# Kernel optimization log

Measured on AMD Instinct MI355X. Metric: run time of the kernel, lower is better.

## Reference

```python
import jax, jax.numpy as jnp
import numpy as np

B, C, H, W = 16, 256, 32, 32
AD, SC, R = 16, 32, 4


def _conv1x1(x, w, b):
    # x: [B,Cin,H,W], w: [Cout,Cin], b: [Cout]
    return jnp.einsum('oc,bchw->bohw', w, x) + b[None, :, None, None]


def setup_inputs() -> dict:
    key = jax.random.key(0)
    ks = jax.random.split(key, 12)
    p = lambda k, shape: (jax.random.normal(k, shape, dtype=jnp.float32) * 0.02)
    return {
        'x': jax.random.normal(ks[0], (B, C, H, W), dtype=jnp.float32),
        'fc1_w': p(ks[1], (C // R, C)), 'fc1_b': jnp.zeros((C // R,), jnp.float32),
        'fc2_w': p(ks[2], (C, C // R)), 'fc2_b': jnp.zeros((C,), jnp.float32),
        'qkv_w': p(ks[3], (AD * 2 + SC, SC)), 'qkv_b': jnp.zeros((AD * 2 + SC,), jnp.float32),
        'proj_w': p(ks[4], (SC, SC)), 'proj_b': jnp.zeros((SC,), jnp.float32),
        'ffn1_w': p(ks[5], (4 * C, C)), 'ffn1_b': jnp.zeros((4 * C,), jnp.float32),
        'ffn2_w': p(ks[6], (C, 4 * C)), 'ffn2_b': jnp.zeros((C,), jnp.float32),
    }


def reference(x, fc1_w, fc1_b, fc2_w, fc2_b, qkv_w, qkv_b, proj_w, proj_b,
              ffn1_w, ffn1_b, ffn2_w, ffn2_b):
    # --- DynamicChannelSelect: SE gate then channel split ---
    s = x.mean(axis=(2, 3), keepdims=True)                       # [B,C,1,1]
    s = jax.nn.relu(_conv1x1(s, fc1_w, fc1_b))
    s = jax.nn.sigmoid(_conv1x1(s, fc2_w, fc2_b))
    xg = x * s
    attn_part, non_attn_part = xg[:, :SC], xg[:, SC:]

    # --- SHSA: single-head self-attention on SC channels ---
    qkv = _conv1x1(attn_part, qkv_w, qkv_b)                      # [B,2*AD+SC,H,W]
    q = qkv[:, :AD].reshape(B, AD, H * W)
    k = qkv[:, AD:2 * AD].reshape(B, AD, H * W)
    v = qkv[:, 2 * AD:].reshape(B, SC, H * W)
    scale = AD ** -0.5
    attn = jax.nn.softmax(jnp.einsum('bcn,bcm->bnm', q, k) * scale, axis=-1)  # [B,N,N]
    out = jnp.einsum('bcm,bnm->bcn', v, attn).reshape(B, SC, H, W)
    attn_out = _conv1x1(out, proj_w, proj_b)

    # --- concat + 1x1-conv FFN ---
    y = jnp.concatenate([attn_out, non_attn_part], axis=1)       # [B,C,H,W]
    h = jax.nn.relu(_conv1x1(y, ffn1_w, ffn1_b))                 # [B,4C,H,W]
    return _conv1x1(h, ffn2_w, ffn2_b)                           # [B,C,H,W]
```

## Files before the change

kernel.cpp:

```cpp
#include <hip/hip_runtime.h>
#include <cstdint>
#include <cstddef>

#define BB 16
#define CC 256
#define NP 1024

typedef __attribute__((ext_vector_type(8))) short bf16x8;
typedef __attribute__((ext_vector_type(4))) float f32x4;
typedef unsigned short u16;

__device__ __forceinline__ u16 f2bf(float f) {
    union { float f; uint32_t u; } v; v.f = f;
    uint32_t u = v.u;
    return (u16)((u + 0x7FFFu + ((u >> 16) & 1u)) >> 16);
}

__global__ __launch_bounds__(256)
void se_mean_conv_kernel(const float* __restrict__ x, float* __restrict__ s_mean,
                         const float* __restrict__ w1, u16* __restrict__ d1,
                         const float* __restrict__ w2, u16* __restrict__ d2) {
    int blk = blockIdx.x;
    int t = threadIdx.x;
    if (blk < BB * CC) {
        const float* p = x + (size_t)blk * NP;
        float4 v = *(const float4*)(p + t * 4);
        float s = (v.x + v.y) + (v.z + v.w);
#pragma unroll
        for (int off = 32; off; off >>= 1) s += __shfl_down(s, off, 64);
        __shared__ float red[4];
        if ((t & 63) == 0) red[t >> 6] = s;
        __syncthreads();
        if (t == 0) s_mean[blk] = (red[0] + red[1] + red[2] + red[3]) * (1.0f / NP);
    } else {
        int blk2 = blk - BB * CC;
        const float* src = (blk2 < 256) ? w1 : w2;
        u16* dst = (blk2 < 256) ? d1 : d2;
        int i = ((blk2 & 255) * 256 + t) * 4;
        float4 v = *(const float4*)(src + i);
        ushort4 o;
        o.x = f2bf(v.x); o.y = f2bf(v.y); o.z = f2bf(v.z); o.w = f2bf(v.w);
        *(ushort4*)(dst + i) = o;
    }
}

__global__ __launch_bounds__(256)
void scale_transpose_qkv_kernel(const float* __restrict__ x, const float* __restrict__ s_mean,
                                const float* __restrict__ fc1_w, const float* __restrict__ fc1_b,
                                const float* __restrict__ fc2_w, const float* __restrict__ fc2_b,
                                const float* __restrict__ qW, const float* __restrict__ qB,
                                u16* __restrict__ ygt, u16* __restrict__ Qt,
                                u16* __restrict__ Kt, u16* __restrict__ Vb) {
    int nt = blockIdx.x, ct = blockIdx.y, b = blockIdx.z;
    __shared__ float tile[64][65];
    __shared__ float ws[64 * 32];
    __shared__ float bs[64];
    __shared__ float vtile[32][64];
    __shared__ float smean_s[CC];
    __shared__ float h1[64];
    __shared__ float sig_l[64];
    int t = threadIdx.x;
    const float* Xb = x + ((size_t)b * CC + ct * 64) * NP + nt * 64;
    smean_s[t] = s_mean[b * CC + t];
    if (ct == 0) {
        for (int e = t; e < 2048; e += 256) ws[e] = qW[e];
        if (t < 64) bs[t] = qB[t];
    }
#pragma unroll
    for (int p = 0; p < 4; ++p) {
        int e = t + p * 256;
        int c = e >> 4, n4 = (e & 15) * 4;
        float4 v = *(const float4*)&Xb[(size_t)c * NP + n4];
        tile[c][n4] = v.x; tile[c][n4 + 1] = v.y; tile[c][n4 + 2] = v.z; tile[c][n4 + 3] = v.w;
    }
    __syncthreads();
    if (t < 64) {
        float a = fc1_b[t];
#pragma unroll 4
        for (int c = 0; c < CC; ++c) a += fc1_w[t * CC + c] * smean_s[c];
        h1[t] = fmaxf(a, 0.f);
    }
    __syncthreads();
    if (t < 64) {
        int c = ct * 64 + t;
        float a = fc2_b[c];
#pragma unroll 8
        for (int j = 0; j < 64; ++j) a += fc2_w[c * 64 + j] * h1[j];
        sig_l[t] = 1.f / (1.f + __expf(-a));
    }
    __syncthreads();
    u16* Yb = ygt + ((size_t)b * NP + nt * 64) * CC + ct * 64;
#pragma unroll
    for (int p = 0; p < 4; ++p) {
        int e = t + p * 256;
        int n = e >> 4, c4 = (e & 15) * 4;
        if (ct * 64 + c4 >= 32) {
            ushort4 o;
            o.x = f2bf(tile[c4][n] * sig_l[c4]);
            o.y = f2bf(tile[c4 + 1][n] * sig_l[c4 + 1]);
            o.z = f2bf(tile[c4 + 2][n] * sig_l[c4 + 2]);
            o.w = f2bf(tile[c4 + 3][n] * sig_l[c4 + 3]);
            *(ushort4*)&Yb[(size_t)n * CC + c4] = o;
        }
    }
    if (ct == 0) {
        int nn = t & 63, g = t >> 6;
        int n = nt * 64 + nn;
        float xs[32];
#pragma unroll
        for (int c = 0; c < 32; ++c) xs[c] = tile[c][nn] * sig_l[c];
        float acc[16];
#pragma unroll
        for (int oc = 0; oc < 16; ++oc) {
            int o = g * 16 + oc;
            float a = bs[o];
#pragma unroll
            for (int c = 0; c < 32; ++c) a += ws[o * 32 + c] * xs[c];
            acc[oc] = a;
        }
        if (g == 0) {
            u16* qr = Qt + ((size_t)b * NP + n) * 32;
            ushort4 z4; z4.x = 0; z4.y = 0; z4.z = 0; z4.w = 0;
#pragma unroll
            for (int j = 0; j < 16; j += 4) {
                ushort4 o4;
                o4.x = f2bf(acc[j] * 0.25f);     o4.y = f2bf(acc[j + 1] * 0.25f);
                o4.z = f2bf(acc[j + 2] * 0.25f); o4.w = f2bf(acc[j + 3] * 0.25f);
                *(ushort4*)&qr[j] = o4;
            }
            *(ushort4*)&qr[16] = z4; *(ushort4*)&qr[20] = z4;
            *(ushort4*)&qr[24] = z4; *(ushort4*)&qr[28] = z4;
        } else if (g == 1) {
            u16* kr = Kt + ((size_t)b * NP + n) * 32;
            ushort4 z4; z4.x = 0; z4.y = 0; z4.z = 0; z4.w = 0;
#pragma unroll
            for (int j = 0; j < 16; j += 4) {
                ushort4 k4;
                k4.x = f2bf(acc[j]);     k4.y = f2bf(acc[j + 1]);
                k4.z = f2bf(acc[j + 2]); k4.w = f2bf(acc[j + 3]);
                *(ushort4*)&kr[j] = k4;
            }
            *(ushort4*)&kr[16] = z4; *(ushort4*)&kr[20] = z4;
            *(ushort4*)&kr[24] = z4; *(ushort4*)&kr[28] = z4;
        } else {
#pragma unroll
            for (int oc = 0; oc < 16; ++oc) vtile[(g - 2) * 16 + oc][nn] = acc[oc];
        }
        __syncthreads();
        for (int e = t; e < 2048; e += 256) {
            int c = e >> 6, nn2 = e & 63;
            Vb[(size_t)b * 32 * NP + (size_t)c * NP + nt * 64 + nn2] = f2bf(vtile[c][nn2]);
        }
    }
}

__global__ __launch_bounds__(256)
void attn_mfma_kernel(const u16* __restrict__ Qt, const u16* __restrict__ Kt,
                      const u16* __restrict__ Vb,
                      const float* __restrict__ proj_w, const float* __restrict__ proj_b,
                      u16* __restrict__ ygt) {
    int b = blockIdx.x & 15;
    int n0 = (blockIdx.x >> 4) * 16;
    __shared__ __align__(16) u16 P_lds[4][16][40];
    __shared__ float al_lds[4][16];
    __shared__ float sm_lds[4][16];
    __shared__ float sl_lds[4][16];
    __shared__ float O_lds[4][16][33];
    __shared__ float pw_s[32][32];
    __shared__ float pb_s[32];
    int t = threadIdx.x;
    int w = t >> 6, lane = t & 63;
    int q = lane >> 4, idx = lane & 15;

    for (int e = t; e < 1024; e += 256) pw_s[e >> 5][e & 31] = proj_w[e];
    if (t < 32) pb_s[t] = proj_b[t];
    __syncthreads();

    const u16* Qb = Qt + (size_t)b * NP * 32;
    const u16* Kb = Kt + (size_t)b * NP * 32;
    const u16* Vp = Vb + (size_t)b * 32 * NP;

    int nrow = n0 + idx;
    bf16x8 aq = *(const bf16x8*)&Qb[(size_t)nrow * 32 + q * 8];

    f32x4 O0 = {0.f, 0.f, 0.f, 0.f}, O1 = {0.f, 0.f, 0.f, 0.f};
    float m_run[4] = {-1e30f, -1e30f, -1e30f, -1e30f};
    float l_run[4] = {0.f, 0.f, 0.f, 0.f};

    int mbase = w * 256;
    for (int m0 = mbase; m0 < mbase + 256; m0 += 32) {
        bf16x8 bk0 = *(const bf16x8*)&Kb[(size_t)(m0 + idx) * 32 + q * 8];
        bf16x8 bk1 = *(const bf16x8*)&Kb[(size_t)(m0 + 16 + idx) * 32 + q * 8];
        bf16x8 va0 = *(const bf16x8*)&Vp[(size_t)idx * NP + m0 + q * 8];
        bf16x8 va1 = *(const bf16x8*)&Vp[(size_t)(16 + idx) * NP + m0 + q * 8];
        f32x4 z = {0.f, 0.f, 0.f, 0.f};
        f32x4 S0 = __builtin_amdgcn_mfma_f32_16x16x32_bf16(aq, bk0, z, 0, 0, 0);
        f32x4 S1 = __builtin_amdgcn_mfma_f32_16x16x32_bf16(aq, bk1, z, 0, 0, 0);
        float mx[4], p0[4], p1[4], alpha[4];
#pragma unroll
        for (int r = 0; r < 4; ++r) mx[r] = fmaxf(S0[r], S1[r]);
#pragma unroll
        for (int off = 1; off < 16; off <<= 1)
#pragma unroll
            for (int r = 0; r < 4; ++r) mx[r] = fmaxf(mx[r], __shfl_xor(mx[r], off, 64));
#pragma unroll
        for (int r = 0; r < 4; ++r) {
            float nm = fmaxf(m_run[r], mx[r]);
            alpha[r] = __expf(m_run[r] - nm);
            m_run[r] = nm;
            p0[r] = __expf(S0[r] - nm);
            p1[r] = __expf(S1[r] - nm);
        }
#pragma unroll
        for (int r = 0; r < 4; ++r) {
            float s = p0[r] + p1[r];
#pragma unroll
            for (int off = 1; off < 16; off <<= 1) s += __shfl_xor(s, off, 64);
            l_run[r] = l_run[r] * alpha[r] + s;
        }
#pragma unroll
        for (int r = 0; r < 4; ++r) {
            P_lds[w][q * 4 + r][idx]      = f2bf(p0[r]);
            P_lds[w][q * 4 + r][idx + 16] = f2bf(p1[r]);
        }
        if (idx == 0) {
#pragma unroll
            for (int r = 0; r < 4; ++r) al_lds[w][q * 4 + r] = alpha[r];
        }
        float an = al_lds[w][idx];
#pragma unroll
        for (int r = 0; r < 4; ++r) { O0[r] *= an; O1[r] *= an; }
        bf16x8 pf = *(const bf16x8*)&P_lds[w][idx][q * 8];
        O0 = __builtin_amdgcn_mfma_f32_16x16x32_bf16(va0, pf, O0, 0, 0, 0);
        O1 = __builtin_amdgcn_mfma_f32_16x16x32_bf16(va1, pf, O1, 0, 0, 0);
    }
    if (idx == 0) {
#pragma unroll
        for (int r = 0; r < 4; ++r) {
            sm_lds[w][q * 4 + r] = m_run[r];
            sl_lds[w][q * 4 + r] = l_run[r];
        }
    }
#pragma unroll
    for (int r = 0; r < 4; ++r) {
        O_lds[w][idx][q * 4 + r]      = O0[r];
        O_lds[w][idx][q * 4 + r + 16] = O1[r];
    }
    __syncthreads();
    if (w == 0) {
        float m0_ = sm_lds[0][idx], m1 = sm_lds[1][idx], m2 = sm_lds[2][idx], m3 = sm_lds[3][idx];
        float gm = fmaxf(fmaxf(m0_, m1), fmaxf(m2, m3));
        float e0 = __expf(m0_ - gm), e1 = __expf(m1 - gm);
        float e2 = __expf(m2 - gm), e3 = __expf(m3 - gm);
        float linv = 1.f / (sl_lds[0][idx] * e0 + sl_lds[1][idx] * e1 +
                            sl_lds[2][idx] * e2 + sl_lds[3][idx] * e3);
#pragma unroll
        for (int r = 0; r < 4; ++r) {
            int c0 = q * 4 + r;
            O_lds[0][idx][c0] = (O_lds[0][idx][c0] * e0 + O_lds[1][idx][c0] * e1 +
                                 O_lds[2][idx][c0] * e2 + O_lds[3][idx][c0] * e3) * linv;
            int c1 = c0 + 16;
            O_lds[0][idx][c1] = (O_lds[0][idx][c1] * e0 + O_lds[1][idx][c1] * e1 +
                                 O_lds[2][idx][c1] * e2 + O_lds[3][idx][c1] * e3) * linv;
        }
        float o0[4], o1[4];
#pragma unroll
        for (int r = 0; r < 4; ++r) { o0[r] = pb_s[q * 4 + r]; o1[r] = pb_s[q * 4 + r + 16]; }
#pragma unroll
        for (int c = 0; c < 32; ++c) {
            float xv = O_lds[0][idx][c];
#pragma unroll
            for (int r = 0; r < 4; ++r) {
                o0[r] += pw_s[q * 4 + r][c] * xv;
                o1[r] += pw_s[q * 4 + r + 16][c] * xv;
            }
        }
        u16* yrow = ygt + ((size_t)b * NP + n0 + idx) * CC;
        ushort4 w0, w1;
        w0.x = f2bf(o0[0]); w0.y = f2bf(o0[1]); w0.z = f2bf(o0[2]); w0.w = f2bf(o0[3]);
        w1.x = f2bf(o1[0]); w1.y = f2bf(o1[1]); w1.z = f2bf(o1[2]); w1.w = f2bf(o1[3]);
        *(ushort4*)&yrow[q * 4] = w0;
        *(ushort4*)&yrow[q * 4 + 16] = w1;
    }
}

template <int K>
__global__ __launch_bounds__(256)
void mfma_gemm_kernel(const u16* __restrict__ A, const u16* __restrict__ Bt,
                      const float* __restrict__ bias, u16* __restrict__ Y, int M) {
    __shared__ __align__(16) u16 As[2][128][64];
    __shared__ __align__(16) u16 Bs[2][128][64];
    constexpr int NIT = K / 64;
    int id = blockIdx.x;
    int xcd = id & 7, qq = id >> 3;
    int mt = qq >> 4;
    int nt = ((qq & 15) << 3) | xcd;
    const u16* Ab = A + (size_t)mt * 128 * K;
    const u16* Bb = Bt + (size_t)nt * 128 * K;
    int t = threadIdx.x;
    int w = t >> 6, lane = t & 63;
    int q = lane >> 4, idx = lane & 15;
    int wr = (w >> 1) * 64, wc = (w & 1) * 64;
    int srow = lane >> 3;
    int gch = (lane & 7) ^ srow;

    f32x4 acc[4][4];
#pragma unroll
    for (int i = 0; i < 4; ++i)
#pragma unroll
        for (int j = 0; j < 4; ++j) { f32x4 z = {0.f, 0.f, 0.f, 0.f}; acc[i][j] = z; }

#define ISSUE_LOADS(buf, k0)                                                              \
    {                                                                                     \
        _Pragma("unroll")                                                                 \
        for (int p = 0; p < 4; ++p) {                                                     \
            int r = w * 32 + p * 8 + srow;                                                \
            __builtin_amdgcn_global_load_lds(                                             \
                (const __attribute__((address_space(1))) void*)(Ab + (size_t)r * K + (k0) + gch * 8), \
                (__attribute__((address_space(3))) void*)(&As[buf][w * 32 + p * 8][0]),   \
                16, 0, 0);                                                                \
        }                                                                                 \
        _Pragma("unroll")                                                                 \
        for (int p = 0; p < 4; ++p) {                                                     \
            int r = w * 32 + p * 8 + srow;                                                \
            __builtin_amdgcn_global_load_lds(                                             \
                (const __attribute__((address_space(1))) void*)(Bb + (size_t)r * K + (k0) + gch * 8), \
                (__attribute__((address_space(3))) void*)(&Bs[buf][w * 32 + p * 8][0]),   \
                16, 0, 0);                                                                \
        }                                                                                 \
    }

    ISSUE_LOADS(0, 0)
    for (int ki = 0; ki < NIT; ++ki) {
        int cur = ki & 1;
        __syncthreads();
        if (ki + 1 < NIT) ISSUE_LOADS(cur ^ 1, (ki + 1) * 64)
#pragma unroll
        for (int h = 0; h < 2; ++h) {
            bf16x8 af[4], bfr[4];
#pragma unroll
            for (int i = 0; i < 4; ++i)
                af[i] = *(const bf16x8*)&As[cur][wr + i * 16 + idx][(((q + 4 * h) ^ (idx & 7)) * 8)];
#pragma unroll
            for (int j = 0; j < 4; ++j)
                bfr[j] = *(const bf16x8*)&Bs[cur][wc + j * 16 + idx][(((q + 4 * h) ^ (idx & 7)) * 8)];
#pragma unroll
            for (int i = 0; i < 4; ++i)
#pragma unroll
                for (int j = 0; j < 4; ++j)
                    acc[i][j] = __builtin_amdgcn_mfma_f32_16x16x32_bf16(af[i], bfr[j], acc[i][j], 0, 0, 0);
        }
    }
#undef ISSUE_LOADS

    __syncthreads();
    u16* tile = &As[0][0][0];
#pragma unroll
    for (int i = 0; i < 4; ++i) {
        int m0 = wr + i * 16 + q * 4;
        int gm = mt * 128 + m0;
        float b0 = bias[gm], b1 = bias[gm + 1], b2 = bias[gm + 2], b3 = bias[gm + 3];
        int c16 = m0 >> 3;
        int off = (q & 1) * 4;
#pragma unroll
        for (int j = 0; j < 4; ++j) {
            int nl = wc + j * 16 + idx;
            f32x4 v = acc[i][j];
            ushort4 o;
            o.x = f2bf(fmaxf(v.x + b0, 0.f)); o.y = f2bf(fmaxf(v.y + b1, 0.f));
            o.z = f2bf(fmaxf(v.z + b2, 0.f)); o.w = f2bf(fmaxf(v.w + b3, 0.f));
            int cs = c16 ^ (nl & 7);
            *(ushort4*)&tile[nl * 128 + cs * 8 + off] = o;
        }
    }
    __syncthreads();
#pragma unroll
    for (int p = 0; p < 8; ++p) {
        int flat = p * 256 + t;
        int n = flat >> 4, c = flat & 15;
        int cs = c ^ (n & 7);
        bf16x8 v = *(const bf16x8*)&tile[n * 128 + cs * 8];
        *(bf16x8*)&Y[((size_t)(nt * 128 + n)) * (size_t)M + mt * 128 + c * 8] = v;
    }
}

template <int K>
__global__ __launch_bounds__(256)
void mfma_gemm_64_kernel(const u16* __restrict__ A, const u16* __restrict__ Bt,
                         const float* __restrict__ bias, float* __restrict__ Y, int M) {
    __shared__ __align__(16) u16 As[2][64][64];
    __shared__ __align__(16) u16 Bs[2][64][64];
    constexpr int NIT = K / 64;
    int id = blockIdx.x;
    int xcd = id & 7, u = id >> 3;
    int mt = u >> 5;
    int j  = (u >> 1) & 15;
    int p_ = u & 1;
    int nt = (((j << 3) | xcd) << 1) | p_;
    const u16* Ab = A + (size_t)mt * 64 * K;
    const u16* Bb = Bt + (size_t)nt * 64 * K;
    int t = threadIdx.x;
    int w = t >> 6, lane = t & 63;
    int q = lane >> 4, idx = lane & 15;
    int wr = (w >> 1) * 32, wc = (w & 1) * 32;
    int srow = lane >> 3;
    int gch = (lane & 7) ^ srow;

    f32x4 acc[2][2];
#pragma unroll
    for (int i = 0; i < 2; ++i)
#pragma unroll
        for (int jj = 0; jj < 2; ++jj) { f32x4 z = {0.f, 0.f, 0.f, 0.f}; acc[i][jj] = z; }

#define ISSUE_LOADS64(buf, k0)                                                            \
    {                                                                                     \
        _Pragma("unroll")                                                                 \
        for (int p = 0; p < 2; ++p) {                                                     \
            int r = w * 16 + p * 8 + srow;                                                \
            __builtin_amdgcn_global_load_lds(                                             \
                (const __attribute__((address_space(1))) void*)(Ab + (size_t)r * K + (k0) + gch * 8), \
                (__attribute__((address_space(3))) void*)(&As[buf][w * 16 + p * 8][0]),   \
                16, 0, 0);                                                                \
        }                                                                                 \
        _Pragma("unroll")                                                                 \
        for (int p = 0; p < 2; ++p) {                                                     \
            int r = w * 16 + p * 8 + srow;                                                \
            __builtin_amdgcn_global_load_lds(                                             \
                (const __attribute__((address_space(1))) void*)(Bb + (size_t)r * K + (k0) + gch * 8), \
                (__attribute__((address_space(3))) void*)(&Bs[buf][w * 16 + p * 8][0]),   \
                16, 0, 0);                                                                \
        }                                                                                 \
    }

    ISSUE_LOADS64(0, 0)
    for (int ki = 0; ki < NIT; ++ki) {
        int cur = ki & 1;
        __syncthreads();
        if (ki + 1 < NIT) ISSUE_LOADS64(cur ^ 1, (ki + 1) * 64)
#pragma unroll
        for (int h = 0; h < 2; ++h) {
            bf16x8 af[2], bfr[2];
#pragma unroll
            for (int i = 0; i < 2; ++i)
                af[i] = *(const bf16x8*)&As[cur][wr + i * 16 + idx][(((q + 4 * h) ^ (idx & 7)) * 8)];
#pragma unroll
            for (int jj = 0; jj < 2; ++jj)
                bfr[jj] = *(const bf16x8*)&Bs[cur][wc + jj * 16 + idx][(((q + 4 * h) ^ (idx & 7)) * 8)];
#pragma unroll
            for (int i = 0; i < 2; ++i)
#pragma unroll
                for (int jj = 0; jj < 2; ++jj)
                    acc[i][jj] = __builtin_amdgcn_mfma_f32_16x16x32_bf16(af[i], bfr[jj], acc[i][jj], 0, 0, 0);
        }
    }
#undef ISSUE_LOADS64

#pragma unroll
    for (int i = 0; i < 2; ++i) {
        int m0 = mt * 64 + wr + i * 16 + q * 4;
        float b0 = bias[m0], b1 = bias[m0 + 1], b2 = bias[m0 + 2], b3 = bias[m0 + 3];
#pragma unroll
        for (int jj = 0; jj < 2; ++jj) {
            int ng = nt * 64 + wc + jj * 16 + idx;
            int bb = ng >> 10, nn = ng & 1023;
            f32x4 v = acc[i][jj];
            float* p = Y + ((size_t)bb * M + m0) * NP + nn;
            p[0]      = v.x + b0;
            p[NP]     = v.y + b1;
            p[2 * NP] = v.z + b2;
            p[3 * NP] = v.w + b3;
        }
    }
}

extern "C" void kernel_launch(void* const* d_in, const int* in_sizes, int n_in,
                              void* d_out, int out_size, void* d_ws, size_t ws_size,
                              hipStream_t stream) {
    const float* x      = (const float*)d_in[0];
    const float* fc1_w  = (const float*)d_in[1];
    const float* fc1_b  = (const float*)d_in[2];
    const float* fc2_w  = (const float*)d_in[3];
    const float* fc2_b  = (const float*)d_in[4];
    const float* qkv_w  = (const float*)d_in[5];
    const float* qkv_b  = (const float*)d_in[6];
    const float* proj_w = (const float*)d_in[7];
    const float* proj_b = (const float*)d_in[8];
    const float* ffn1_w = (const float*)d_in[9];
    const float* ffn1_b = (const float*)d_in[10];
    const float* ffn2_w = (const float*)d_in[11];
    const float* ffn2_b = (const float*)d_in[12];
    float* out = (float*)d_out;

    u16* w1b = (u16*)d_ws;
    u16* w2b = w1b + 262144;
    u16* ygt = w2b + 262144;
    u16* ht  = ygt + (size_t)BB * NP * CC;
    float* s_mean = (float*)ht;
    u16* Qt = (u16*)(s_mean + BB * CC);
    u16* Kt = Qt + (size_t)BB * NP * 32;
    u16* Vb = Kt + (size_t)BB * NP * 32;

    se_mean_conv_kernel<<<BB * CC + 512, 256, 0, stream>>>(x, s_mean, ffn1_w, w1b, ffn2_w, w2b);
    scale_transpose_qkv_kernel<<<dim3(16, 4, BB), 256, 0, stream>>>(
        x, s_mean, fc1_w, fc1_b, fc2_w, fc2_b, qkv_w, qkv_b, ygt, Qt, Kt, Vb);
    attn_mfma_kernel<<<BB * 64, 256, 0, stream>>>(Qt, Kt, Vb, proj_w, proj_b, ygt);

    mfma_gemm_kernel<256><<<1024, 256, 0, stream>>>(w1b, ygt, ffn1_b, ht, 1024);
    mfma_gemm_64_kernel<1024><<<1024, 256, 0, stream>>>(w2b, ht, ffn2_b, out, 256);
}
```

Baseline: 170.8 us.

## Fuse the two FFN GEMMs into one kernel keeping hidden activations in LDS

The separate FFN1 and FFN2 GEMM kernels are replaced by one fused kernel. Each block owns 64 pixels, computes the 1024-wide hidden layer in 64-channel chunks into double-buffered LDS, and accumulates the FFN2 output in registers. This removes the global write and re-read of the 32 MB bf16 hidden tensor and one launch. In exchange only 256 blocks run, weights are read straight from global/L2 into registers with no LDS staging, and each chunk needs a block barrier, so occupancy and latency hiding may suffer.

```diff
diff --git a/kernel.cpp b/kernel.cpp
--- a/kernel.cpp
+++ b/kernel.cpp
@@ -284,191 +284,112 @@
     }
 }
 
-template <int K>
 __global__ __launch_bounds__(256)
-void mfma_gemm_kernel(const u16* __restrict__ A, const u16* __restrict__ Bt,
-                      const float* __restrict__ bias, u16* __restrict__ Y, int M) {
-    __shared__ __align__(16) u16 As[2][128][64];
-    __shared__ __align__(16) u16 Bs[2][128][64];
-    constexpr int NIT = K / 64;
-    int id = blockIdx.x;
-    int xcd = id & 7, qq = id >> 3;
-    int mt = qq >> 4;
-    int nt = ((qq & 15) << 3) | xcd;
-    const u16* Ab = A + (size_t)mt * 128 * K;
-    const u16* Bb = Bt + (size_t)nt * 128 * K;
+void ffn_fused_kernel(const u16* __restrict__ w1b, const u16* __restrict__ w2b,
+                      const u16* __restrict__ ygt,
+                      const float* __restrict__ bias1, const float* __restrict__ bias2,
+                      float* __restrict__ out) {
+    __shared__ __align__(16) u16 Ys[4][64][64];
+    __shared__ __align__(16) u16 Hs[2][64][64];
+    __shared__ float Bs1[1024];
     int t = threadIdx.x;
     int w = t >> 6, lane = t & 63;
     int q = lane >> 4, idx = lane & 15;
-    int wr = (w >> 1) * 64, wc = (w & 1) * 64;
     int srow = lane >> 3;
     int gch = (lane & 7) ^ srow;
-
-    f32x4 acc[4][4];
-#pragma unroll
-    for (int i = 0; i < 4; ++i)
-#pragma unroll
-        for (int j = 0; j < 4; ++j) { f32x4 z = {0.f, 0.f, 0.f, 0.f}; acc[i][j] = z; }
-
-#define ISSUE_LOADS(buf, k0)                                                              \
-    {                                                                                     \
-        _Pragma("unroll")                                                                 \
-        for (int p = 0; p < 4; ++p) {                                                     \
-            int r = w * 32 + p * 8 + srow;                                                \
-            __builtin_amdgcn_global_load_lds(                                             \
-                (const __attribute__((address_space(1))) void*)(Ab + (size_t)r * K + (k0) + gch * 8), \
-                (__attribute__((address_space(3))) void*)(&As[buf][w * 32 + p * 8][0]),   \
-                16, 0, 0);                                                                \
-        }                                                                                 \
-        _Pragma("unroll")                                                                 \
-        for (int p = 0; p < 4; ++p) {                                                     \
-            int r = w * 32 + p * 8 + srow;                                                \
-            __builtin_amdgcn_global_load_lds(                                             \
-                (const __attribute__((address_space(1))) void*)(Bb + (size_t)r * K + (k0) + gch * 8), \
-                (__attribute__((address_space(3))) void*)(&Bs[buf][w * 32 + p * 8][0]),   \
-                16, 0, 0);                                                                \
-        }                                                                                 \
-    }
-
-    ISSUE_LOADS(0, 0)
-    for (int ki = 0; ki < NIT; ++ki) {
-        int cur = ki & 1;
+    int n0 = blockIdx.x * 64;
+
+#pragma unroll
+    for (int p = 0; p < 8; ++p) {
+        int kb = p >> 1;
+        int nb = (p & 1) * 32 + w * 8;
+        __builtin_amdgcn_global_load_lds(
+            (const __attribute__((address_space(1))) void*)(ygt + (size_t)(n0 + nb + srow) * CC + kb * 64 + gch * 8),
+            (__attribute__((address_space(3))) void*)(&Ys[kb][nb][0]),
+            16, 0, 0);
+    }
+    for (int e = t; e < 1024; e += 256) Bs1[e] = bias1[e];
+
+    f32x4 oacc[4][4];
+#pragma unroll
+    for (int f = 0; f < 4; ++f)
+#pragma unroll
+        for (int j = 0; j < 4; ++j) { f32x4 z = {0.f, 0.f, 0.f, 0.f}; oacc[f][j] = z; }
+
+    __syncthreads();
+
+    bf16x8 af[8];
+    {
+        const u16* a1 = w1b + ((size_t)(w * 16 + idx)) * CC;
+#pragma unroll
+        for (int s = 0; s < 8; ++s) af[s] = *(const bf16x8*)(a1 + s * 32 + q * 8);
+    }
+
+    for (int ch = 0; ch < 16; ++ch) {
+        bf16x8 af2[4][2];
+        const u16* a2 = w2b + ((size_t)(w * 64 + idx)) * 1024 + ch * 64;
+#pragma unroll
+        for (int f = 0; f < 4; ++f)
+#pragma unroll
+            for (int s2 = 0; s2 < 2; ++s2)
+                af2[f][s2] = *(const bf16x8*)(a2 + (size_t)f * 16 * 1024 + s2 * 32 + q * 8);
+
+        f32x4 hacc[4];
+#pragma unroll
+        for (int j = 0; j < 4; ++j) { f32x4 z = {0.f, 0.f, 0.f, 0.f}; hacc[j] = z; }
+#pragma unroll
+        for (int s = 0; s < 8; ++s) {
+            int kb = s >> 1, hh = s & 1;
+#pragma unroll
+            for (int j = 0; j < 4; ++j) {
+                bf16x8 yb = *(const bf16x8*)&Ys[kb][j * 16 + idx][(((q + 4 * hh) ^ (idx & 7)) * 8)];
+                hacc[j] = __builtin_amdgcn_mfma_f32_16x16x32_bf16(af[s], yb, hacc[j], 0, 0, 0);
+            }
+        }
+        int mbase = ch * 64 + w * 16 + q * 4;
+        float b0 = Bs1[mbase], b1v = Bs1[mbase + 1], b2v = Bs1[mbase + 2], b3v = Bs1[mbase + 3];
+        int chk_hi = w * 2 + (q >> 1);
+#pragma unroll
+        for (int j = 0; j < 4; ++j) {
+            int n = j * 16 + idx;
+            int chk = chk_hi ^ (n & 7);
+            uint32_t lo = (uint32_t)f2bf(fmaxf(hacc[j][0] + b0, 0.f)) |
+                          ((uint32_t)f2bf(fmaxf(hacc[j][1] + b1v, 0.f)) << 16);
+            uint32_t hi = (uint32_t)f2bf(fmaxf(hacc[j][2] + b2v, 0.f)) |
+                          ((uint32_t)f2bf(fmaxf(hacc[j][3] + b3v, 0.f)) << 16);
+            uint32_t* hp = (uint32_t*)&Hs[ch & 1][n][chk * 8 + (q & 1) * 4];
+            hp[0] = lo; hp[1] = hi;
+        }
         __syncthreads();
-        if (ki + 1 < NIT) ISSUE_LOADS(cur ^ 1, (ki + 1) * 64)
-#pragma unroll
-        for (int h = 0; h < 2; ++h) {
-            bf16x8 af[4], bfr[4];
-#pragma unroll
-            for (int i = 0; i < 4; ++i)
-                af[i] = *(const bf16x8*)&As[cur][wr + i * 16 + idx][(((q + 4 * h) ^ (idx & 7)) * 8)];
-#pragma unroll
-            for (int j = 0; j < 4; ++j)
-                bfr[j] = *(const bf16x8*)&Bs[cur][wc + j * 16 + idx][(((q + 4 * h) ^ (idx & 7)) * 8)];
-#pragma unroll
-            for (int i = 0; i < 4; ++i)
-#pragma unroll
-                for (int j = 0; j < 4; ++j)
-                    acc[i][j] = __builtin_amdgcn_mfma_f32_16x16x32_bf16(af[i], bfr[j], acc[i][j], 0, 0, 0);
-        }
-    }
-#undef ISSUE_LOADS
-
-    __syncthreads();
-    u16* tile = &As[0][0][0];
-#pragma unroll
-    for (int i = 0; i < 4; ++i) {
-        int m0 = wr + i * 16 + q * 4;
-        int gm = mt * 128 + m0;
-        float b0 = bias[gm], b1 = bias[gm + 1], b2 = bias[gm + 2], b3 = bias[gm + 3];
-        int c16 = m0 >> 3;
-        int off = (q & 1) * 4;
+        if (ch + 1 < 16) {
+            const u16* a1 = w1b + ((size_t)((ch + 1) * 64 + w * 16 + idx)) * CC;
+#pragma unroll
+            for (int s = 0; s < 8; ++s) af[s] = *(const bf16x8*)(a1 + s * 32 + q * 8);
+        }
+#pragma unroll
+        for (int s2 = 0; s2 < 2; ++s2)
+#pragma unroll
+            for (int j = 0; j < 4; ++j) {
+                bf16x8 hb = *(const bf16x8*)&Hs[ch & 1][j * 16 + idx][(((q + 4 * s2) ^ (idx & 7)) * 8)];
+#pragma unroll
+                for (int f = 0; f < 4; ++f)
+                    oacc[f][j] = __builtin_amdgcn_mfma_f32_16x16x32_bf16(af2[f][s2], hb, oacc[f][j], 0, 0, 0);
+            }
+    }
+
+    int b = n0 >> 10, nnb = n0 & 1023;
+#pragma unroll
+    for (int f = 0; f < 4; ++f) {
+        int m2 = w * 64 + f * 16 + q * 4;
+        float c0 = bias2[m2], c1 = bias2[m2 + 1], c2 = bias2[m2 + 2], c3 = bias2[m2 + 3];
 #pragma unroll
         for (int j = 0; j < 4; ++j) {
-            int nl = wc + j * 16 + idx;
-            f32x4 v = acc[i][j];
-            ushort4 o;
-            o.x = f2bf(fmaxf(v.x + b0, 0.f)); o.y = f2bf(fmaxf(v.y + b1, 0.f));
-            o.z = f2bf(fmaxf(v.z + b2, 0.f)); o.w = f2bf(fmaxf(v.w + b3, 0.f));
-            int cs = c16 ^ (nl & 7);
-            *(ushort4*)&tile[nl * 128 + cs * 8 + off] = o;
-        }
-    }
-    __syncthreads();
-#pragma unroll
-    for (int p = 0; p < 8; ++p) {
-        int flat = p * 256 + t;
-        int n = flat >> 4, c = flat & 15;
-        int cs = c ^ (n & 7);
-        bf16x8 v = *(const bf16x8*)&tile[n * 128 + cs * 8];
-        *(bf16x8*)&Y[((size_t)(nt * 128 + n)) * (size_t)M + mt * 128 + c * 8] = v;
-    }
-}
-
-template <int K>
-__global__ __launch_bounds__(256)
-void mfma_gemm_64_kernel(const u16* __restrict__ A, const u16* __restrict__ Bt,
-                         const float* __restrict__ bias, float* __restrict__ Y, int M) {
-    __shared__ __align__(16) u16 As[2][64][64];
-    __shared__ __align__(16) u16 Bs[2][64][64];
-    constexpr int NIT = K / 64;
-    int id = blockIdx.x;
-    int xcd = id & 7, u = id >> 3;
-    int mt = u >> 5;
-    int j  = (u >> 1) & 15;
-    int p_ = u & 1;
-    int nt = (((j << 3) | xcd) << 1) | p_;
-    const u16* Ab = A + (size_t)mt * 64 * K;
-    const u16* Bb = Bt + (size_t)nt * 64 * K;
-    int t = threadIdx.x;
-    int w = t >> 6, lane = t & 63;
-    int q = lane >> 4, idx = lane & 15;
-    int wr = (w >> 1) * 32, wc = (w & 1) * 32;
-    int srow = lane >> 3;
-    int gch = (lane & 7) ^ srow;
-
-    f32x4 acc[2][2];
-#pragma unroll
-    for (int i = 0; i < 2; ++i)
-#pragma unroll
-        for (int jj = 0; jj < 2; ++jj) { f32x4 z = {0.f, 0.f, 0.f, 0.f}; acc[i][jj] = z; }
-
-#define ISSUE_LOADS64(buf, k0)                                                            \
-    {                                                                                     \
-        _Pragma("unroll")                                                                 \
-        for (int p = 0; p < 2; ++p) {                                                     \
-            int r = w * 16 + p * 8 + srow;                                                \
-            __builtin_amdgcn_global_load_lds(                                             \
-                (const __attribute__((address_space(1))) void*)(Ab + (size_t)r * K + (k0) + gch * 8), \
-                (__attribute__((address_space(3))) void*)(&As[buf][w * 16 + p * 8][0]),   \
-                16, 0, 0);                                                                \
-        }                                                                                 \
-        _Pragma("unroll")                                                                 \
-        for (int p = 0; p < 2; ++p) {                                                     \
-            int r = w * 16 + p * 8 + srow;                                                \
-            __builtin_amdgcn_global_load_lds(                                             \
-                (const __attribute__((address_space(1))) void*)(Bb + (size_t)r * K + (k0) + gch * 8), \
-                (__attribute__((address_space(3))) void*)(&Bs[buf][w * 16 + p * 8][0]),   \
-                16, 0, 0);                                                                \
-        }                                                                                 \
-    }
-
-    ISSUE_LOADS64(0, 0)
-    for (int ki = 0; ki < NIT; ++ki) {
-        int cur = ki & 1;
-        __syncthreads();
-        if (ki + 1 < NIT) ISSUE_LOADS64(cur ^ 1, (ki + 1) * 64)
-#pragma unroll
-        for (int h = 0; h < 2; ++h) {
-            bf16x8 af[2], bfr[2];
-#pragma unroll
-            for (int i = 0; i < 2; ++i)
-                af[i] = *(const bf16x8*)&As[cur][wr + i * 16 + idx][(((q + 4 * h) ^ (idx & 7)) * 8)];
-#pragma unroll
-            for (int jj = 0; jj < 2; ++jj)
-                bfr[jj] = *(const bf16x8*)&Bs[cur][wc + jj * 16 + idx][(((q + 4 * h) ^ (idx & 7)) * 8)];
-#pragma unroll
-            for (int i = 0; i < 2; ++i)
-#pragma unroll
-                for (int jj = 0; jj < 2; ++jj)
-                    acc[i][jj] = __builtin_amdgcn_mfma_f32_16x16x32_bf16(af[i], bfr[jj], acc[i][jj], 0, 0, 0);
-        }
-    }
-#undef ISSUE_LOADS64
-
-#pragma unroll
-    for (int i = 0; i < 2; ++i) {
-        int m0 = mt * 64 + wr + i * 16 + q * 4;
-        float b0 = bias[m0], b1 = bias[m0 + 1], b2 = bias[m0 + 2], b3 = bias[m0 + 3];
-#pragma unroll
-        for (int jj = 0; jj < 2; ++jj) {
-            int ng = nt * 64 + wc + jj * 16 + idx;
-            int bb = ng >> 10, nn = ng & 1023;
-            f32x4 v = acc[i][jj];
-            float* p = Y + ((size_t)bb * M + m0) * NP + nn;
-            p[0]      = v.x + b0;
-            p[NP]     = v.y + b1;
-            p[2 * NP] = v.z + b2;
-            p[3 * NP] = v.w + b3;
+            float* p = out + ((size_t)b * CC + m2) * NP + nnb + j * 16 + idx;
+            f32x4 v = oacc[f][j];
+            p[0]      = v.x + c0;
+            p[NP]     = v.y + c1;
+            p[2 * NP] = v.z + c2;
+            p[3 * NP] = v.w + c3;
         }
     }
 }
@@ -494,8 +415,8 @@
     u16* w1b = (u16*)d_ws;
     u16* w2b = w1b + 262144;
     u16* ygt = w2b + 262144;
-    u16* ht  = ygt + (size_t)BB * NP * CC;
-    float* s_mean = (float*)ht;
+    u16* scratch = ygt + (size_t)BB * NP * CC;
+    float* s_mean = (float*)scratch;
     u16* Qt = (u16*)(s_mean + BB * CC);
     u16* Kt = Qt + (size_t)BB * NP * 32;
     u16* Vb = Kt + (size_t)BB * NP * 32;
@@ -505,6 +426,5 @@
         x, s_mean, fc1_w, fc1_b, fc2_w, fc2_b, qkv_w, qkv_b, ygt, Qt, Kt, Vb);
     attn_mfma_kernel<<<BB * 64, 256, 0, stream>>>(Qt, Kt, Vb, proj_w, proj_b, ygt);
 
-    mfma_gemm_kernel<256><<<1024, 256, 0, stream>>>(w1b, ygt, ffn1_b, ht, 1024);
-    mfma_gemm_64_kernel<1024><<<1024, 256, 0, stream>>>(w2b, ht, ffn2_b, out, 256);
-}
+    ffn_fused_kernel<<<256, 256, 0, stream>>>(w1b, w2b, ygt, ffn1_b, ffn2_b, out);
+}
```

Result: no change. 172.5 us (+1.0%).
